# Kernel optimization log

Hardware: AMD Instinct MI355X
Metric: run time of the kernel (lower is better)

Reference implementation:

```python
import jax, jax.numpy as jnp
import numpy as np

AGENT_RADIUS = 0.5
SAFETY_DIST = 0.1
QP_ITERS = 300


def _qp_solve(p, G, h):
    """Batched QP: min_u 0.5 u^T u + p^T u  s.t.  G u <= h  (Q = I).
    Solved in the dual by projected gradient ascent (differentiable, fixed iters).
    p: [B,2], G: [B,m,2], h: [B,m] -> u: [B,2]
    """
    GGt = jnp.einsum('bmi,bni->bmn', G, G)                 # [B,m,m]
    q = jnp.einsum('bmi,bi->bm', G, p) + h                 # [B,m]
    # Lipschitz upper bound per sample (Frobenius norm of GG^T)
    L = jnp.sqrt(jnp.sum(GGt * GGt, axis=(1, 2))) + 1e-6   # [B]
    alpha = (1.0 / L)[:, None]

    def step(lam, _):
        grad = jnp.einsum('bmn,bn->bm', GGt, lam) + q
        lam = jnp.maximum(lam - alpha * grad, 0.0)
        return lam, None

    lam0 = jnp.zeros_like(h)
    lam, _ = jax.lax.scan(step, lam0, None, length=QP_ITERS)
    u = -p - jnp.einsum('bmi,bm->bi', G, lam)
    return u


def setup_inputs() -> dict:
    key = jax.random.key(0)
    ks = jax.random.split(key, 20)
    B, F, H1, H2 = 8192, 8, 1024, 512

    def w(k, i, o):
        return (jax.random.normal(k, (i, o), jnp.float32) / np.sqrt(i)).astype(jnp.float32)

    obs_xy = jax.random.uniform(ks[17], (8, 2), jnp.float32, -10.0, 10.0)
    obs_r = jax.random.uniform(ks[18], (8, 1), jnp.float32, 0.3, 0.8)
    return {
        'x': jax.random.normal(ks[0], (B, F), jnp.float32),
        'mean': 0.1 * jax.random.normal(ks[1], (F,), jnp.float32),
        'std': jax.random.uniform(ks[2], (F,), jnp.float32, 0.5, 1.5),
        'W1': w(ks[3], F, H1), 'b1': jnp.zeros((H1,), jnp.float32),
        'W21': w(ks[4], H1, H2), 'b21': jnp.zeros((H2,), jnp.float32),
        'W22': w(ks[5], H1, H2), 'b22': jnp.zeros((H2,), jnp.float32),
        'W23': w(ks[6], H1, H2), 'b23': jnp.zeros((H2,), jnp.float32),
        'W31': w(ks[7], H2, 2), 'b31': jnp.zeros((2,), jnp.float32),
        'W32': w(ks[8], H2, 2), 'b32': jnp.zeros((2,), jnp.float32),
        'W33': w(ks[9], H2, 1), 'b33': jnp.zeros((1,), jnp.float32),
        'obstacles': jnp.concatenate([obs_xy, obs_r], axis=1),  # [8,3] (x,y,r)
        'sgn': 1,
    }


def reference(x, mean, std, W1, b1, W21, b21, W22, b22, W23, b23,
              W31, b31, W32, b32, W33, b33, obstacles, sgn):
    B = x.shape[0]
    x0 = x * std + mean                                   # un-normalized state [B,8]

    h1 = jax.nn.relu(x @ W1 + b1)
    x21 = jax.nn.relu(h1 @ W21 + b21)
    x22 = jax.nn.relu(h1 @ W22 + b22)
    x23 = jax.nn.relu(h1 @ W23 + b23)
    x31 = x21 @ W31 + b31                                 # QP linear term p [B,2]
    x32 = 4.0 * jax.nn.sigmoid(x22 @ W32 + b32)           # CBF gains p1,p2 [B,2]
    x33 = 4.0 * jax.nn.sigmoid(x23 @ W33 + b33)           # liveness gain (unused, smg off)

    px, py, theta, v = x0[:, 0], x0[:, 1], x0[:, 2], x0[:, 3]
    st, ct = jnp.sin(theta)[:, None], jnp.cos(theta)[:, None]
    vb = v[:, None]

    # static obstacles broadcast to batch + opponent as last obstacle -> [B, m]
    ox = jnp.concatenate([jnp.broadcast_to(obstacles[:, 0][None], (B, obstacles.shape[0])), x0[:, 4:5]], axis=1)
    oy = jnp.concatenate([jnp.broadcast_to(obstacles[:, 1][None], (B, obstacles.shape[0])), x0[:, 5:6]], axis=1)
    orad = jnp.concatenate([jnp.broadcast_to(obstacles[:, 2][None], (B, obstacles.shape[0])),
                            jnp.full((B, 1), AGENT_RADIUS, x0.dtype)], axis=1)

    R = AGENT_RADIUS + orad + SAFETY_DIST
    dx = px[:, None] - ox                                  # [B,m]
    dy = py[:, None] - oy

    barrier = dx * dx + dy * dy - R * R
    barrier_dot = 2.0 * dx * vb * ct + 2.0 * dy * vb * st
    Lf2b = (2.0 * v * v)[:, None]
    LgLfbu1 = -2.0 * dx * vb * st + 2.0 * dy * vb * ct
    LgLfbu2 = 2.0 * dx * ct + 2.0 * dy * st
    G = jnp.stack([-LgLfbu1, -LgLfbu2], axis=-1)           # [B,m,2]
    p1, p2 = x32[:, 0:1], x32[:, 1:2]
    h = Lf2b + (p1 + p2) * barrier_dot + p1 * p2 * barrier # [B,m]

    u = _qp_solve(x31, G, h)                               # [B,2]
    return u
```

## Files before the change

### kernel.cpp

```cpp
#include <hip/hip_runtime.h>
#include <cstdint>
#include <cstddef>

typedef unsigned short u16;
typedef u16   u16x8  __attribute__((ext_vector_type(8)));
typedef u16   u16x4  __attribute__((ext_vector_type(4)));
typedef __bf16 bf16x8 __attribute__((ext_vector_type(8)));
typedef float f32x4  __attribute__((ext_vector_type(4)));
typedef float f32x2  __attribute__((ext_vector_type(2)));

__device__ __forceinline__ float bf2f(u16 v) {
  unsigned int u = ((unsigned int)v) << 16;
  return __builtin_bit_cast(float, u);
}
__device__ __forceinline__ u16 f2bf(float f) {
  unsigned int x = __builtin_bit_cast(unsigned int, f);
  x += 0x7fffu + ((x >> 16) & 1u);
  return (u16)(x >> 16);
}

__device__ __forceinline__ void gld_lds16(const u16* g, u16* l) {
  __builtin_amdgcn_global_load_lds(
      (const __attribute__((address_space(1))) unsigned int*)g,
      (__attribute__((address_space(3))) unsigned int*)l, 16, 0, 0);
}

__global__ __launch_bounds__(256) void k_prep(const float* __restrict__ W21,
                                              const float* __restrict__ W22,
                                              u16* __restrict__ Wt,
                                              const float* __restrict__ x,
                                              const float* __restrict__ W1,
                                              const float* __restrict__ b1,
                                              u16* __restrict__ h1,
                                              float* __restrict__ head) {
  __shared__ u16 s[64][65];
  const int b = blockIdx.x;
  if (b < 256) {
    const int mat = b >> 7;
    const int tt  = b & 127;
    const int k0  = (tt >> 3) * 64;
    const int n0  = (tt & 7) * 64;
    const float* W = mat ? W22 : W21;
    const int tx = threadIdx.x & 63;
    const int ty = threadIdx.x >> 6;
#pragma unroll
    for (int i = 0; i < 16; ++i) {
      int r = i * 4 + ty;
      s[r][tx] = f2bf(W[(size_t)(k0 + r) * 512 + n0 + tx]);
    }
    __syncthreads();
    const int nbase = mat * 512 + n0;
#pragma unroll
    for (int i = 0; i < 16; ++i) {
      int r = i * 4 + ty;
      Wt[(size_t)(nbase + r) * 1024 + k0 + tx] = s[tx][r];
    }
  } else {
    const int row0 = (b - 256) * 8;
    if (threadIdx.x < 8)
      *(f32x4*)(head + 4 * (size_t)(row0 + threadIdx.x)) = f32x4{0.f, 0.f, 0.f, 0.f};
    const int c4 = threadIdx.x * 4;
    f32x4 bv = *(const f32x4*)(b1 + c4);
    f32x4 acc[8];
#pragma unroll
    for (int r = 0; r < 8; ++r) acc[r] = bv;
#pragma unroll
    for (int f = 0; f < 8; ++f) {
      f32x4 wv = *(const f32x4*)(W1 + f * 1024 + c4);
#pragma unroll
      for (int r = 0; r < 8; ++r) {
        float xv = x[(size_t)(row0 + r) * 8 + f];
#pragma unroll
        for (int e = 0; e < 4; ++e) acc[r][e] = fmaf(xv, wv[e], acc[r][e]);
      }
    }
#pragma unroll
    for (int r = 0; r < 8; ++r) {
      u16x4 o;
#pragma unroll
      for (int e = 0; e < 4; ++e) o[e] = f2bf(fmaxf(acc[r][e], 0.f));
      *(u16x4*)(h1 + (size_t)(row0 + r) * 1024 + c4) = o;
    }
  }
}

__global__ __launch_bounds__(256) void k_gemm(const u16* __restrict__ A,
                                              const u16* __restrict__ Bt,
                                              const float* __restrict__ b21,
                                              const float* __restrict__ b22,
                                              const float* __restrict__ W31,
                                              const float* __restrict__ W32,
                                              float* __restrict__ head) {
  constexpr int K  = 1024;
  constexpr int BK = 64;
  constexpr int NT = K / BK;
  __shared__ u16 As[2][128 * 64];
  __shared__ u16 Bs[2][128 * 64];

  const int t    = threadIdx.x;
  const int row0 = blockIdx.x * 128;
  const int col0 = blockIdx.y * 128;
  const int w    = t >> 6;
  const int lane = t & 63;
  const int wr   = w >> 1, wc = w & 1;
  const int lrow = lane & 15;
  const int kq   = lane >> 4;

  const u16* gA[4];
  const u16* gB[4];
  int lo[4];
#pragma unroll
  for (int m = 0; m < 4; ++m) {
    const int s  = t + 256 * m;
    const int gc = (s & 7) ^ ((s >> 3) & 7);
    gA[m] = A  + (size_t)(row0 + (s >> 3)) * K + gc * 8;
    gB[m] = Bt + (size_t)(col0 + (s >> 3)) * K + gc * 8;
    lo[m] = s * 8;
  }
  const int po0 = (((0 * 4) + kq) ^ (lrow & 7)) * 8;
  const int po1 = (((1 * 4) + kq) ^ (lrow & 7)) * 8;

  f32x4 acc[4][4];
#pragma unroll
  for (int i = 0; i < 4; ++i)
#pragma unroll
    for (int j = 0; j < 4; ++j) acc[i][j] = f32x4{0.f, 0.f, 0.f, 0.f};

#pragma unroll
  for (int m = 0; m < 4; ++m) {
    gld_lds16(gA[m], As[0] + lo[m]);
    gld_lds16(gB[m], Bs[0] + lo[m]);
  }

  for (int kt = 0; kt < NT; ++kt) {
    const int cur = kt & 1, nxt = cur ^ 1;
    __syncthreads();

    if (kt + 1 < NT) {
      const int ko = (kt + 1) * BK;
#pragma unroll
      for (int m = 0; m < 4; ++m) {
        gld_lds16(gA[m] + ko, As[nxt] + lo[m]);
        gld_lds16(gB[m] + ko, Bs[nxt] + lo[m]);
      }
    }

#pragma unroll
    for (int s32 = 0; s32 < 2; ++s32) {
      const int po = s32 ? po1 : po0;
      bf16x8 af[4], bfr[4];
#pragma unroll
      for (int i = 0; i < 4; ++i)
        af[i] = __builtin_bit_cast(bf16x8,
            *(const u16x8*)(As[cur] + (wr * 64 + i * 16 + lrow) * 64 + po));
#pragma unroll
      for (int j = 0; j < 4; ++j)
        bfr[j] = __builtin_bit_cast(bf16x8,
            *(const u16x8*)(Bs[cur] + (wc * 64 + j * 16 + lrow) * 64 + po));
#pragma unroll
      for (int i = 0; i < 4; ++i)
#pragma unroll
        for (int j = 0; j < 4; ++j)
          acc[i][j] = __builtin_amdgcn_mfma_f32_16x16x32_bf16(af[i], bfr[j], acc[i][j], 0, 0, 0);
    }
  }

  const bool isX21 = (col0 < 512);
  const float* Wh  = isX21 ? W31 : W32;
  const int   hoff = isX21 ? 0 : 2;

  float hx[16], hy[16];
#pragma unroll
  for (int n = 0; n < 16; ++n) { hx[n] = 0.f; hy[n] = 0.f; }
#pragma unroll
  for (int j = 0; j < 4; ++j) {
    int col  = col0 + wc * 64 + j * 16 + lrow;
    int wcol = col & 511;
    f32x2 wv = *(const f32x2*)(Wh + 2 * wcol);
    float bias = isX21 ? b21[col] : b22[wcol];
#pragma unroll
    for (int i = 0; i < 4; ++i)
#pragma unroll
      for (int rr = 0; rr < 4; ++rr) {
        float v = fmaxf(acc[i][j][rr] + bias, 0.f);
        hx[i * 4 + rr] = fmaf(v, wv[0], hx[i * 4 + rr]);
        hy[i * 4 + rr] = fmaf(v, wv[1], hy[i * 4 + rr]);
      }
  }
#pragma unroll
  for (int m = 1; m <= 8; m <<= 1) {
#pragma unroll
    for (int n = 0; n < 16; ++n) {
      hx[n] += __shfl_xor(hx[n], m, 64);
      hy[n] += __shfl_xor(hy[n], m, 64);
    }
  }
  if (lrow == 0) {
#pragma unroll
    for (int i = 0; i < 4; ++i)
#pragma unroll
      for (int rr = 0; rr < 4; ++rr) {
        int row = row0 + wr * 64 + i * 16 + kq * 4 + rr;
        atomicAdd(head + 4 * (size_t)row + hoff,     hx[i * 4 + rr]);
        atomicAdd(head + 4 * (size_t)row + hoff + 1, hy[i * 4 + rr]);
      }
  }
}

__global__ __launch_bounds__(256) void k_qp(const float* __restrict__ x,
                                            const float* __restrict__ mean_,
                                            const float* __restrict__ std_,
                                            const float* __restrict__ head,
                                            const float* __restrict__ b31,
                                            const float* __restrict__ b32,
                                            const float* __restrict__ obstacles,
                                            float* __restrict__ out) {
  const int r = blockIdx.x * 256 + threadIdx.x;
  f32x4 hd = *(const f32x4*)(head + 4 * (size_t)r);
  float p0  = hd[0] + b31[0];
  float p1v = hd[1] + b31[1];
  float pp1 = 4.f / (1.f + expf(-(hd[2] + b32[0])));
  float pp2 = 4.f / (1.f + expf(-(hd[3] + b32[1])));

  const f32x4* xp = (const f32x4*)(x + (size_t)r * 8);
  f32x4 xa = xp[0], xb = xp[1];
  float px = xa[0] * std_[0] + mean_[0];
  float py = xa[1] * std_[1] + mean_[1];
  float th = xa[2] * std_[2] + mean_[2];
  float v  = xa[3] * std_[3] + mean_[3];
  float ax = xb[0] * std_[4] + mean_[4];
  float ay = xb[1] * std_[5] + mean_[5];
  float st = sinf(th), ct = cosf(th);
  float Lf2b = 2.f * v * v;

  float G0[9], G1[9], q[9];
  float s00 = 0.f, s01 = 0.f, s11 = 0.f;
#pragma unroll
  for (int m = 0; m < 9; ++m) {
    float ox, oy, orad;
    if (m < 8) {
      ox = obstacles[m * 3]; oy = obstacles[m * 3 + 1]; orad = obstacles[m * 3 + 2];
    } else { ox = ax; oy = ay; orad = 0.5f; }
    float R  = 0.6f + orad;
    float dx = px - ox, dy = py - oy;
    float bar  = dx * dx + dy * dy - R * R;
    float dct  = dx * ct + dy * st;
    float bdot = 2.f * v * dct;
    float g0 = 2.f * v * (dx * st - dy * ct);
    float g1 = -2.f * dct;
    float h  = Lf2b + (pp1 + pp2) * bdot + pp1 * pp2 * bar;
    G0[m] = g0; G1[m] = g1;
    q[m] = g0 * p0 + g1 * p1v + h;
    s00 += g0 * g0; s01 += g0 * g1; s11 += g1 * g1;
  }
  float L = sqrtf(s00 * s00 + 2.f * s01 * s01 + s11 * s11) + 1e-6f;
  float alpha = 1.f / L;

  f32x2 G0p[4], G1p[4], qp2[4], lamp[4];
#pragma unroll
  for (int j = 0; j < 4; ++j) {
    G0p[j] = f32x2{G0[j], G0[j + 4]};
    G1p[j] = f32x2{G1[j], G1[j + 4]};
    qp2[j] = f32x2{q[j],  q[j + 4]};
    lamp[j] = f32x2{0.f, 0.f};
  }
  float G08 = G0[8], G18 = G1[8], q8 = q[8], lam8 = 0.f;
  const f32x2 nav = {-alpha, -alpha};
  const f32x2 z2  = {0.f, 0.f};

  for (int it = 0; it < 300; ++it) {
    f32x2 pv0[4], pv1[4];
#pragma unroll
    for (int j = 0; j < 4; ++j) {
      pv0[j] = G0p[j] * lamp[j];
      pv1[j] = G1p[j] * lamp[j];
    }
    float pr08 = G08 * lam8, pr18 = G18 * lam8;
    f32x2 c0 = (pv0[0] + pv0[1]) + (pv0[2] + pv0[3]);
    f32x2 c1 = (pv1[0] + pv1[1]) + (pv1[2] + pv1[3]);
    float t0 = (c0.x + c0.y) + pr08;
    float t1 = (c1.x + c1.y) + pr18;
    f32x2 t0v = {t0, t0}, t1v = {t1, t1};
#pragma unroll
    for (int j = 0; j < 4; ++j) {
      f32x2 g = __builtin_elementwise_fma(G0p[j], t0v,
                __builtin_elementwise_fma(G1p[j], t1v, qp2[j]));
      lamp[j] = __builtin_elementwise_max(
                __builtin_elementwise_fma(nav, g, lamp[j]), z2);
    }
    float g8 = fmaf(G08, t0, fmaf(G18, t1, q8));
    lam8 = fmaxf(fmaf(-alpha, g8, lam8), 0.f);
  }

  float u0 = -p0, u1 = -p1v;
#pragma unroll
  for (int j = 0; j < 4; ++j) {
    u0 = fmaf(-G0p[j].x, lamp[j].x, u0);
    u1 = fmaf(-G1p[j].x, lamp[j].x, u1);
  }
#pragma unroll
  for (int j = 0; j < 4; ++j) {
    u0 = fmaf(-G0p[j].y, lamp[j].y, u0);
    u1 = fmaf(-G1p[j].y, lamp[j].y, u1);
  }
  u0 = fmaf(-G08, lam8, u0);
  u1 = fmaf(-G18, lam8, u1);
  *(f32x2*)(out + 2 * (size_t)r) = f32x2{u0, u1};
}

extern "C" void kernel_launch(void* const* d_in, const int* in_sizes, int n_in,
                              void* d_out, int out_size, void* d_ws, size_t ws_size,
                              hipStream_t stream) {
  const float* x    = (const float*)d_in[0];
  const float* mean_= (const float*)d_in[1];
  const float* std_ = (const float*)d_in[2];
  const float* W1   = (const float*)d_in[3];
  const float* b1   = (const float*)d_in[4];
  const float* W21  = (const float*)d_in[5];
  const float* b21  = (const float*)d_in[6];
  const float* W22  = (const float*)d_in[7];
  const float* b22  = (const float*)d_in[8];
  const float* W31  = (const float*)d_in[11];
  const float* b31  = (const float*)d_in[12];
  const float* W32  = (const float*)d_in[13];
  const float* b32  = (const float*)d_in[14];
  const float* obst = (const float*)d_in[17];
  float* out = (float*)d_out;

  char* ws = (char*)d_ws;
  u16*   Wt   = (u16*)ws;
  u16*   h1   = (u16*)(ws + (size_t)(1 << 21));
  float* head = (float*)(ws + (size_t)(1 << 21) + (size_t)(1 << 24));

  k_prep<<<256 + 1024, 256, 0, stream>>>(W21, W22, Wt, x, W1, b1, h1, head);
  k_gemm<<<dim3(64, 8), 256, 0, stream>>>(h1, Wt, b21, b22, W31, W32, head);
  k_qp  <<<32, 256, 0, stream>>>(x, mean_, std_, head, b31, b32, obst, out);
}
```

Before: 160.5 us.

## Pre-swizzle GEMM operands into MFMA fragment layout and load directly from global

The prep kernel now writes h1 and the transposed weights in a fragment-major layout, so each lane's 16-byte MFMA operand is contiguous. The GEMM drops LDS staging, double buffering and barriers, and loads fragments straight from global memory into registers. It also uses a 256x128 block tile with 4x8 accumulators per wave. This removes LDS traffic and synchronisation, but depends on L2/cache hit rates and global latency without explicit prefetch, and raises register pressure with fewer blocks.

After: 171.5 us. 6.8% more time.

```diff
diff --git a/kernel.cpp b/kernel.cpp
--- a/kernel.cpp
+++ b/kernel.cpp
@@ -9,201 +9,175 @@
 typedef float f32x4  __attribute__((ext_vector_type(4)));
 typedef float f32x2  __attribute__((ext_vector_type(2)));
 
-__device__ __forceinline__ float bf2f(u16 v) {
-  unsigned int u = ((unsigned int)v) << 16;
-  return __builtin_bit_cast(float, u);
-}
 __device__ __forceinline__ u16 f2bf(float f) {
   unsigned int x = __builtin_bit_cast(unsigned int, f);
   x += 0x7fffu + ((x >> 16) & 1u);
   return (u16)(x >> 16);
 }
 
-__device__ __forceinline__ void gld_lds16(const u16* g, u16* l) {
-  __builtin_amdgcn_global_load_lds(
-      (const __attribute__((address_space(1))) unsigned int*)g,
-      (__attribute__((address_space(3))) unsigned int*)l, 16, 0, 0);
-}
 
 __global__ __launch_bounds__(256) void k_prep(const float* __restrict__ W21,
                                               const float* __restrict__ W22,
-                                              u16* __restrict__ Wt,
+                                              u16* __restrict__ Wtf,
                                               const float* __restrict__ x,
                                               const float* __restrict__ W1,
                                               const float* __restrict__ b1,
-                                              u16* __restrict__ h1,
+                                              u16* __restrict__ h1f,
                                               float* __restrict__ head) {
-  __shared__ u16 s[64][65];
-  const int b = blockIdx.x;
+  __shared__ u16 smem[16 * 1024];
+  const int b  = blockIdx.x;
+  const int t  = threadIdx.x;
+  const int l  = t & 63, wv = t >> 6;
+  const int lrow = l & 15, kq = l >> 4;
+
   if (b < 256) {
+    u16 (*s)[65] = (u16(*)[65])smem;
     const int mat = b >> 7;
     const int tt  = b & 127;
     const int k0  = (tt >> 3) * 64;
     const int n0  = (tt & 7) * 64;
     const float* W = mat ? W22 : W21;
-    const int tx = threadIdx.x & 63;
-    const int ty = threadIdx.x >> 6;
+    const int tx = t & 63;
+    const int ty = t >> 6;
 #pragma unroll
     for (int i = 0; i < 16; ++i) {
       int r = i * 4 + ty;
       s[r][tx] = f2bf(W[(size_t)(k0 + r) * 512 + n0 + tx]);
     }
     __syncthreads();
-    const int nbase = mat * 512 + n0;
-#pragma unroll
-    for (int i = 0; i < 16; ++i) {
-      int r = i * 4 + ty;
-      Wt[(size_t)(nbase + r) * 1024 + k0 + tx] = s[tx][r];
+    const int ntg0  = (mat * 512 + n0) >> 4;
+    const int k32g0 = k0 >> 5;
+#pragma unroll
+    for (int k32l = 0; k32l < 2; ++k32l) {
+      u16x8 v;
+#pragma unroll
+      for (int e = 0; e < 8; ++e)
+        v[e] = s[k32l * 32 + kq * 8 + e][wv * 16 + lrow];
+      *(u16x8*)(Wtf + (size_t)((ntg0 + wv) * 32 + k32g0 + k32l) * 512 + l * 8) = v;
     }
   } else {
-    const int row0 = (b - 256) * 8;
-    if (threadIdx.x < 8)
-      *(f32x4*)(head + 4 * (size_t)(row0 + threadIdx.x)) = f32x4{0.f, 0.f, 0.f, 0.f};
-    const int c4 = threadIdx.x * 4;
+    const int mt    = b - 256;
+    const int row0t = mt * 16;
+    if (t < 16)
+      *(f32x4*)(head + 4 * (size_t)(row0t + t)) = f32x4{0.f, 0.f, 0.f, 0.f};
+    const int c4 = t * 4;
     f32x4 bv = *(const f32x4*)(b1 + c4);
-    f32x4 acc[8];
-#pragma unroll
-    for (int r = 0; r < 8; ++r) acc[r] = bv;
-#pragma unroll
-    for (int f = 0; f < 8; ++f) {
-      f32x4 wv = *(const f32x4*)(W1 + f * 1024 + c4);
-#pragma unroll
-      for (int r = 0; r < 8; ++r) {
-        float xv = x[(size_t)(row0 + r) * 8 + f];
-#pragma unroll
-        for (int e = 0; e < 4; ++e) acc[r][e] = fmaf(xv, wv[e], acc[r][e]);
+    for (int g = 0; g < 2; ++g) {
+      const int row0 = row0t + g * 8;
+      f32x4 acc[8];
+#pragma unroll
+      for (int r = 0; r < 8; ++r) acc[r] = bv;
+#pragma unroll
+      for (int f = 0; f < 8; ++f) {
+        f32x4 wvv = *(const f32x4*)(W1 + f * 1024 + c4);
+#pragma unroll
+        for (int r = 0; r < 8; ++r) {
+          float xv = x[(size_t)(row0 + r) * 8 + f];
+#pragma unroll
+          for (int e = 0; e < 4; ++e) acc[r][e] = fmaf(xv, wvv[e], acc[r][e]);
+        }
       }
-    }
-#pragma unroll
-    for (int r = 0; r < 8; ++r) {
-      u16x4 o;
-#pragma unroll
-      for (int e = 0; e < 4; ++e) o[e] = f2bf(fmaxf(acc[r][e], 0.f));
-      *(u16x4*)(h1 + (size_t)(row0 + r) * 1024 + c4) = o;
-    }
-  }
-}
-
-__global__ __launch_bounds__(256) void k_gemm(const u16* __restrict__ A,
-                                              const u16* __restrict__ Bt,
+#pragma unroll
+      for (int rr = 0; rr < 8; ++rr) {
+        u16x4 o;
+#pragma unroll
+        for (int e = 0; e < 4; ++e) o[e] = f2bf(fmaxf(acc[rr][e], 0.f));
+        const int r  = g * 8 + rr;
+        const int cc = (t >> 1) ^ (r & 7);
+        *(u16x4*)(smem + r * 1024 + cc * 8 + (t & 1) * 4) = o;
+      }
+    }
+    __syncthreads();
+#pragma unroll
+    for (int i = 0; i < 8; ++i) {
+      const int k32 = wv + i * 4;
+      const int cc  = (k32 * 4 + kq) ^ (lrow & 7);
+      u16x8 v = *(const u16x8*)(smem + lrow * 1024 + cc * 8);
+      *(u16x8*)(h1f + (size_t)(mt * 32 + k32) * 512 + l * 8) = v;
+    }
+  }
+}
+
+__global__ __launch_bounds__(256) void k_gemm(const u16* __restrict__ Af,
+                                              const u16* __restrict__ Bf,
                                               const float* __restrict__ b21,
                                               const float* __restrict__ b22,
                                               const float* __restrict__ W31,
                                               const float* __restrict__ W32,
                                               float* __restrict__ head) {
-  constexpr int K  = 1024;
-  constexpr int BK = 64;
-  constexpr int NT = K / BK;
-  __shared__ u16 As[2][128 * 64];
-  __shared__ u16 Bs[2][128 * 64];
-
-  const int t    = threadIdx.x;
-  const int row0 = blockIdx.x * 128;
+  const int t = threadIdx.x, l = t & 63, wv = t >> 6;
+  const int lrow = l & 15, kq = l >> 4;
   const int col0 = blockIdx.y * 128;
-  const int w    = t >> 6;
-  const int lane = t & 63;
-  const int wr   = w >> 1, wc = w & 1;
-  const int lrow = lane & 15;
-  const int kq   = lane >> 4;
-
-  const u16* gA[4];
-  const u16* gB[4];
-  int lo[4];
-#pragma unroll
-  for (int m = 0; m < 4; ++m) {
-    const int s  = t + 256 * m;
-    const int gc = (s & 7) ^ ((s >> 3) & 7);
-    gA[m] = A  + (size_t)(row0 + (s >> 3)) * K + gc * 8;
-    gB[m] = Bt + (size_t)(col0 + (s >> 3)) * K + gc * 8;
-    lo[m] = s * 8;
-  }
-  const int po0 = (((0 * 4) + kq) ^ (lrow & 7)) * 8;
-  const int po1 = (((1 * 4) + kq) ^ (lrow & 7)) * 8;
-
-  f32x4 acc[4][4];
+  const u16* Ab = Af + (size_t)((blockIdx.x * 16 + wv * 4) * 32) * 512 + l * 8;
+  const u16* Bb = Bf + (size_t)((blockIdx.y * 8) * 32) * 512 + l * 8;
+
+  f32x4 acc[4][8];
 #pragma unroll
   for (int i = 0; i < 4; ++i)
 #pragma unroll
-    for (int j = 0; j < 4; ++j) acc[i][j] = f32x4{0.f, 0.f, 0.f, 0.f};
-
-#pragma unroll
-  for (int m = 0; m < 4; ++m) {
-    gld_lds16(gA[m], As[0] + lo[m]);
-    gld_lds16(gB[m], Bs[0] + lo[m]);
-  }
-
-  for (int kt = 0; kt < NT; ++kt) {
-    const int cur = kt & 1, nxt = cur ^ 1;
-    __syncthreads();
-
-    if (kt + 1 < NT) {
-      const int ko = (kt + 1) * BK;
-#pragma unroll
-      for (int m = 0; m < 4; ++m) {
-        gld_lds16(gA[m] + ko, As[nxt] + lo[m]);
-        gld_lds16(gB[m] + ko, Bs[nxt] + lo[m]);
-      }
-    }
-
-#pragma unroll
-    for (int s32 = 0; s32 < 2; ++s32) {
-      const int po = s32 ? po1 : po0;
-      bf16x8 af[4], bfr[4];
-#pragma unroll
-      for (int i = 0; i < 4; ++i)
-        af[i] = __builtin_bit_cast(bf16x8,
-            *(const u16x8*)(As[cur] + (wr * 64 + i * 16 + lrow) * 64 + po));
-#pragma unroll
-      for (int j = 0; j < 4; ++j)
-        bfr[j] = __builtin_bit_cast(bf16x8,
-            *(const u16x8*)(Bs[cur] + (wc * 64 + j * 16 + lrow) * 64 + po));
-#pragma unroll
-      for (int i = 0; i < 4; ++i)
-#pragma unroll
-        for (int j = 0; j < 4; ++j)
-          acc[i][j] = __builtin_amdgcn_mfma_f32_16x16x32_bf16(af[i], bfr[j], acc[i][j], 0, 0, 0);
-    }
+    for (int j = 0; j < 8; ++j) acc[i][j] = f32x4{0.f, 0.f, 0.f, 0.f};
+
+#pragma unroll 2
+  for (int k32 = 0; k32 < 32; ++k32) {
+    bf16x8 af[4], bfr[8];
+#pragma unroll
+    for (int i = 0; i < 4; ++i)
+      af[i] = __builtin_bit_cast(bf16x8,
+          *(const u16x8*)(Ab + (i * 32 + k32) * 512));
+#pragma unroll
+    for (int j = 0; j < 8; ++j)
+      bfr[j] = __builtin_bit_cast(bf16x8,
+          *(const u16x8*)(Bb + (j * 32 + k32) * 512));
+#pragma unroll
+    for (int i = 0; i < 4; ++i)
+#pragma unroll
+      for (int j = 0; j < 8; ++j)
+        acc[i][j] = __builtin_amdgcn_mfma_f32_16x16x32_bf16(af[i], bfr[j], acc[i][j], 0, 0, 0);
   }
 
   const bool isX21 = (col0 < 512);
   const float* Wh  = isX21 ? W31 : W32;
   const int   hoff = isX21 ? 0 : 2;
 
-  float hx[16], hy[16];
-#pragma unroll
-  for (int n = 0; n < 16; ++n) { hx[n] = 0.f; hy[n] = 0.f; }
-#pragma unroll
-  for (int j = 0; j < 4; ++j) {
-    int col  = col0 + wc * 64 + j * 16 + lrow;
-    int wcol = col & 511;
-    f32x2 wv = *(const f32x2*)(Wh + 2 * wcol);
-    float bias = isX21 ? b21[col] : b22[wcol];
-#pragma unroll
-    for (int i = 0; i < 4; ++i)
-#pragma unroll
-      for (int rr = 0; rr < 4; ++rr) {
-        float v = fmaxf(acc[i][j][rr] + bias, 0.f);
-        hx[i * 4 + rr] = fmaf(v, wv[0], hx[i * 4 + rr]);
-        hy[i * 4 + rr] = fmaf(v, wv[1], hy[i * 4 + rr]);
+#pragma unroll
+  for (int half = 0; half < 2; ++half) {
+    float hx[16], hy[16];
+#pragma unroll
+    for (int n = 0; n < 16; ++n) { hx[n] = 0.f; hy[n] = 0.f; }
+#pragma unroll
+    for (int jj = 0; jj < 4; ++jj) {
+      const int j    = half * 4 + jj;
+      const int col  = col0 + j * 16 + lrow;
+      const int wcol = col & 511;
+      f32x2 wvv = *(const f32x2*)(Wh + 2 * wcol);
+      float bias = isX21 ? b21[col] : b22[wcol];
+#pragma unroll
+      for (int i = 0; i < 4; ++i)
+#pragma unroll
+        for (int rr = 0; rr < 4; ++rr) {
+          float v = fmaxf(acc[i][j][rr] + bias, 0.f);
+          hx[i * 4 + rr] = fmaf(v, wvv[0], hx[i * 4 + rr]);
+          hy[i * 4 + rr] = fmaf(v, wvv[1], hy[i * 4 + rr]);
+        }
+    }
+#pragma unroll
+    for (int m = 1; m <= 8; m <<= 1) {
+#pragma unroll
+      for (int n = 0; n < 16; ++n) {
+        hx[n] += __shfl_xor(hx[n], m, 64);
+        hy[n] += __shfl_xor(hy[n], m, 64);
       }
-  }
-#pragma unroll
-  for (int m = 1; m <= 8; m <<= 1) {
-#pragma unroll
-    for (int n = 0; n < 16; ++n) {
-      hx[n] += __shfl_xor(hx[n], m, 64);
-      hy[n] += __shfl_xor(hy[n], m, 64);
-    }
-  }
-  if (lrow == 0) {
-#pragma unroll
-    for (int i = 0; i < 4; ++i)
-#pragma unroll
-      for (int rr = 0; rr < 4; ++rr) {
-        int row = row0 + wr * 64 + i * 16 + kq * 4 + rr;
-        atomicAdd(head + 4 * (size_t)row + hoff,     hx[i * 4 + rr]);
-        atomicAdd(head + 4 * (size_t)row + hoff + 1, hy[i * 4 + rr]);
-      }
+    }
+    if (lrow == 0) {
+#pragma unroll
+      for (int i = 0; i < 4; ++i)
+#pragma unroll
+        for (int rr = 0; rr < 4; ++rr) {
+          int row = blockIdx.x * 256 + wv * 64 + i * 16 + kq * 4 + rr;
+          atomicAdd(head + 4 * (size_t)row + hoff,     hx[i * 4 + rr]);
+          atomicAdd(head + 4 * (size_t)row + hoff + 1, hy[i * 4 + rr]);
+        }
+    }
   }
 }
 
@@ -328,11 +302,11 @@
   float* out = (float*)d_out;
 
   char* ws = (char*)d_ws;
-  u16*   Wt   = (u16*)ws;
-  u16*   h1   = (u16*)(ws + (size_t)(1 << 21));
+  u16*   Wtf  = (u16*)ws;
+  u16*   h1f  = (u16*)(ws + (size_t)(1 << 21));
   float* head = (float*)(ws + (size_t)(1 << 21) + (size_t)(1 << 24));
 
-  k_prep<<<256 + 1024, 256, 0, stream>>>(W21, W22, Wt, x, W1, b1, h1, head);
-  k_gemm<<<dim3(64, 8), 256, 0, stream>>>(h1, Wt, b21, b22, W31, W32, head);
+  k_prep<<<256 + 512, 256, 0, stream>>>(W21, W22, Wtf, x, W1, b1, h1f, head);
+  k_gemm<<<dim3(32, 8), 256, 0, stream>>>(h1f, Wtf, b21, b22, W31, W32, head);
   k_qp  <<<32, 256, 0, stream>>>(x, mean_, std_, head, b31, b32, obst, out);
 }
```
